# Optimization experiments

Hardware: AMD Instinct MI355X
Metric: run time of the kernel (lower is better)

Reference implementation:

```python
import jax, jax.numpy as jnp
import numpy as np

B, NQ, NN, EMB, H, D = 64, 256, 512, 128, 8, 16
SQRT_EMB = float(np.sqrt(EMB))
LOGIT_CLIP = 10.0


def setup_inputs() -> dict:
    key = jax.random.key(0)
    ks = jax.random.split(key, 9)
    encoded_last_node = jax.random.normal(ks[0], (B, NQ, EMB), jnp.float32)
    attr = jax.random.uniform(ks[1], (B, NQ, 1), jnp.float32)  # e.g. remaining load in [0,1]
    encoded_nodes = jax.random.normal(ks[2], (B, NN, EMB), jnp.float32)
    ninf_mask = jnp.where(jax.random.uniform(ks[3], (B, NQ, NN)) < 0.15,
                          -jnp.inf, 0.0).astype(jnp.float32)
    def lin(k, fan_in, fan_out):
        lim = 1.0 / np.sqrt(fan_in)
        return jax.random.uniform(k, (fan_in, fan_out), jnp.float32, -lim, lim)
    Wq_last = lin(ks[4], EMB + 1, H * D)
    Wk = lin(ks[5], EMB, H * D)
    Wv = lin(ks[6], EMB, H * D)
    Wcomb = lin(ks[7], H * D, EMB)
    bcomb = jax.random.uniform(ks[8], (EMB,), jnp.float32, -1.0 / np.sqrt(H * D), 1.0 / np.sqrt(H * D))
    return dict(encoded_last_node=encoded_last_node, attr=attr,
                encoded_nodes=encoded_nodes, ninf_mask=ninf_mask,
                Wq_last=Wq_last, Wk=Wk, Wv=Wv, Wcomb=Wcomb, bcomb=bcomb)


def _heads(x):  # [B, T, H*D] -> [B, H, T, D]
    return x.reshape(x.shape[0], x.shape[1], H, D).transpose(0, 2, 1, 3)


def reference(encoded_last_node, attr, encoded_nodes, ninf_mask,
              Wq_last, Wk, Wv, Wcomb, bcomb):
    # fix fully-masked rows: un-mask index 0 (matches torch mask_inf patch)
    all_inf = jnp.isinf(ninf_mask).all(axis=2)  # [B, NQ]
    ninf_mask = ninf_mask.at[:, :, 0].set(jnp.where(all_inf, 0.0, ninf_mask[:, :, 0]))

    # set_kv
    k = _heads(encoded_nodes @ Wk)  # [B,H,NN,D]
    v = _heads(encoded_nodes @ Wv)  # [B,H,NN,D]

    # q from last node + attr
    q = _heads(jnp.concatenate([encoded_last_node, attr], axis=2) @ Wq_last)  # [B,H,NQ,D]

    # masked multi-head attention
    score = jnp.einsum('bhnd,bhmd->bhnm', q, k) / jnp.sqrt(jnp.float32(D))
    score = score + ninf_mask[:, None, :, :]          # rank3 mask broadcast over heads
    weights = jax.nn.softmax(score, axis=-1)          # [B,H,NQ,NN]
    out = jnp.einsum('bhnm,bhmd->bhnd', weights, v)
    out_concat = out.transpose(0, 2, 1, 3).reshape(B, NQ, H * D)
    mh_atten_out = out_concat @ Wcomb + bcomb         # [B,NQ,EMB]

    # single-head compatibility score + tanh clip + mask + softmax
    score2 = jnp.einsum('bne,bme->bnm', mh_atten_out, encoded_nodes) / SQRT_EMB
    logits = LOGIT_CLIP * jnp.tanh(score2) + ninf_mask
    probs = jax.nn.softmax(logits, axis=2)            # [B,NQ,NN]
    return probs
```

## Files before the change

kernel.cpp:

```cpp
#include <hip/hip_runtime.h>
#include <math.h>

#define NB    64
#define NQn   256
#define NNn   512
#define HDn   128
#define LOG2E 1.44269504088896340736f
#define INV_SQRT_EMB 0.08838834764831845f

__device__ __forceinline__ float4 ldg4(const float* p) {
    return *reinterpret_cast<const float4*>(p);
}

__global__ __launch_bounds__(256, 2)
void proj_kernel(const float* __restrict__ X,
                 const float* __restrict__ W0, const float* __restrict__ W1,
                 const float* __restrict__ wrow, const float* __restrict__ attr,
                 const float* __restrict__ bias,
                 float* __restrict__ Y0, float* __restrict__ Y1)
{
    __shared__ float Xs[64 * 128];
    __shared__ float Wt[64 * 128];
    const int tid = threadIdx.x;
    const int rg = tid >> 4;
    const int cg = tid & 15;
    const int rowblk = blockIdx.x * 64;
    const int colbase = blockIdx.y * 64;

    #pragma unroll
    for (int i = 0; i < 8; ++i) {
        int idx = tid + 256 * i;
        int r = idx >> 5;
        int c4 = idx & 31;
        float4 v = ldg4(X + (rowblk + r) * 128 + c4 * 4);
        *reinterpret_cast<float4*>(&Xs[r * 128 + ((c4 ^ (r & 7)) << 2)]) = v;
    }

    for (int pass = 0; pass < 2; ++pass) {
        if (pass && (W1 == nullptr)) break;
        const float* W = pass ? W1 : W0;
        float* Y = pass ? Y1 : Y0;
        __syncthreads();
        #pragma unroll
        for (int i = 0; i < 32; ++i) {
            int idx = tid + 256 * i;
            int k = idx >> 6;
            int c = idx & 63;
            float w = W[k * 128 + colbase + c];
            Wt[c * 128 + ((((k >> 2) ^ (c & 7)) << 2) | (k & 3))] = w;
        }
        __syncthreads();

        float acc[4][4];
        #pragma unroll
        for (int r = 0; r < 4; ++r)
            #pragma unroll
            for (int c = 0; c < 4; ++c) acc[r][c] = 0.f;

        const int rsw = rg & 7;
        const int csw = cg & 7;
        #pragma unroll 8
        for (int k4 = 0; k4 < 32; ++k4) {
            float4 a[4], bv[4];
            #pragma unroll
            for (int r = 0; r < 4; ++r)
                a[r] = *reinterpret_cast<const float4*>(&Xs[(rg + 16 * r) * 128 + ((k4 ^ rsw) << 2)]);
            #pragma unroll
            for (int c = 0; c < 4; ++c)
                bv[c] = *reinterpret_cast<const float4*>(&Wt[(cg + 16 * c) * 128 + ((k4 ^ csw) << 2)]);
            #pragma unroll
            for (int r = 0; r < 4; ++r)
                #pragma unroll
                for (int c = 0; c < 4; ++c)
                    acc[r][c] += a[r].x * bv[c].x + a[r].y * bv[c].y
                               + a[r].z * bv[c].z + a[r].w * bv[c].w;
        }

        if (attr != nullptr) {
            #pragma unroll
            for (int r = 0; r < 4; ++r) {
                float av = attr[rowblk + rg + 16 * r];
                #pragma unroll
                for (int c = 0; c < 4; ++c)
                    acc[r][c] += av * wrow[colbase + cg + 16 * c];
            }
        }
        #pragma unroll
        for (int r = 0; r < 4; ++r) {
            int row = rowblk + rg + 16 * r;
            #pragma unroll
            for (int c = 0; c < 4; ++c) {
                int col = colbase + cg + 16 * c;
                float o = acc[r][c];
                if (bias != nullptr) o += bias[col];
                Y[row * 128 + col] = o;
            }
        }
    }
}

__global__ __launch_bounds__(512, 4)
void attn_kernel(const float* __restrict__ Q, const float* __restrict__ K,
                 const float* __restrict__ V, const float* __restrict__ mask,
                 float* __restrict__ P0, float* __restrict__ P1,
                 float* __restrict__ L0, float* __restrict__ L1)
{
    __shared__ float Ks[32 * 128];
    __shared__ float Vs[32 * 128];
    __shared__ float Ms[32 * 64];
    const int tid  = threadIdx.x;
    const int lane = tid & 63;
    const int h    = tid >> 6;
    const int b    = blockIdx.x;
    const int qt   = blockIdx.y;
    const int ns   = blockIdx.z;
    const int q    = qt * 64 + lane;
    const int nb   = ns * 256;

    float qv[16];
    {
        const float* qp = Q + (b * NQn + q) * 128 + h * 16;
        const float sc = 0.25f * LOG2E;
        float4 t0 = ldg4(qp), t1 = ldg4(qp + 4), t2 = ldg4(qp + 8), t3 = ldg4(qp + 12);
        qv[0]=t0.x*sc;  qv[1]=t0.y*sc;  qv[2]=t0.z*sc;  qv[3]=t0.w*sc;
        qv[4]=t1.x*sc;  qv[5]=t1.y*sc;  qv[6]=t1.z*sc;  qv[7]=t1.w*sc;
        qv[8]=t2.x*sc;  qv[9]=t2.y*sc;  qv[10]=t2.z*sc; qv[11]=t2.w*sc;
        qv[12]=t3.x*sc; qv[13]=t3.y*sc; qv[14]=t3.z*sc; qv[15]=t3.w*sc;
    }

    float out[16];
    #pragma unroll
    for (int d = 0; d < 16; ++d) out[d] = 0.f;
    float lsum = 0.f;

    const int srow = tid >> 3;
    const int sn4  = tid & 7;

    for (int t = 0; t < 8; ++t) {
        const int n0 = nb + t * 32;
        __syncthreads();
        {
            int i0 = tid, i1 = tid + 512;
            const float* kg = K + (b * NNn + n0) * 128;
            const float* vg = V + (b * NNn + n0) * 128;
            float4 k0 = ldg4(kg + i0 * 4), k1 = ldg4(kg + i1 * 4);
            float4 v0 = ldg4(vg + i0 * 4), v1 = ldg4(vg + i1 * 4);
            float4 mk = ldg4(mask + (b * NQn + qt * 64 + srow) * NNn + n0 + sn4 * 4);
            *reinterpret_cast<float4*>(&Ks[i0 * 4]) = k0;
            *reinterpret_cast<float4*>(&Ks[i1 * 4]) = k1;
            *reinterpret_cast<float4*>(&Vs[i0 * 4]) = v0;
            *reinterpret_cast<float4*>(&Vs[i1 * 4]) = v1;
            float mks[4] = {mk.x, mk.y, mk.z, mk.w};
            #pragma unroll
            for (int j = 0; j < 4; ++j) {
                int n = sn4 * 4 + j;
                Ms[n * 64 + (srow ^ n)] = mks[j];
            }
        }
        __syncthreads();

        const float* kbase = &Ks[h * 16];
        const float* vbase = &Vs[h * 16];
        #pragma unroll 2
        for (int g = 0; g < 8; ++g) {
            float p[4];
            #pragma unroll
            for (int j = 0; j < 4; ++j) {
                const int n = g * 4 + j;
                const float* kr = kbase + n * 128;
                float kf[16];
                *reinterpret_cast<float4*>(&kf[0])  = *reinterpret_cast<const float4*>(kr);
                *reinterpret_cast<float4*>(&kf[4])  = *reinterpret_cast<const float4*>(kr + 4);
                *reinterpret_cast<float4*>(&kf[8])  = *reinterpret_cast<const float4*>(kr + 8);
                *reinterpret_cast<float4*>(&kf[12]) = *reinterpret_cast<const float4*>(kr + 12);
                float mv = Ms[n * 64 + (lane ^ n)];
                float sA = qv[0]*kf[0] + qv[1]*kf[1] + qv[2]*kf[2] + qv[3]*kf[3];
                float sB = qv[4]*kf[4] + qv[5]*kf[5] + qv[6]*kf[6] + qv[7]*kf[7];
                float sC = qv[8]*kf[8] + qv[9]*kf[9] + qv[10]*kf[10] + qv[11]*kf[11];
                float sD = qv[12]*kf[12] + qv[13]*kf[13] + qv[14]*kf[14] + qv[15]*kf[15];
                float s = ((sA + sB) + (sC + sD)) + mv;
                p[j] = exp2f(s);
                lsum += p[j];
            }
            #pragma unroll
            for (int j = 0; j < 4; ++j) {
                const int n = g * 4 + j;
                const float* vr = vbase + n * 128;
                float vf[16];
                *reinterpret_cast<float4*>(&vf[0])  = *reinterpret_cast<const float4*>(vr);
                *reinterpret_cast<float4*>(&vf[4])  = *reinterpret_cast<const float4*>(vr + 4);
                *reinterpret_cast<float4*>(&vf[8])  = *reinterpret_cast<const float4*>(vr + 8);
                *reinterpret_cast<float4*>(&vf[12]) = *reinterpret_cast<const float4*>(vr + 12);
                #pragma unroll
                for (int d = 0; d < 16; ++d) out[d] += p[j] * vf[d];
            }
        }
    }

    float* P = ns ? P1 : P0;
    float* L = ns ? L1 : L0;
    float* op = P + (b * NQn + q) * 128 + h * 16;
    *reinterpret_cast<float4*>(op)      = make_float4(out[0],  out[1],  out[2],  out[3]);
    *reinterpret_cast<float4*>(op + 4)  = make_float4(out[4],  out[5],  out[6],  out[7]);
    *reinterpret_cast<float4*>(op + 8)  = make_float4(out[8],  out[9],  out[10], out[11]);
    *reinterpret_cast<float4*>(op + 12) = make_float4(out[12], out[13], out[14], out[15]);
    L[(b * NQn + q) * 8 + h] = lsum;
}

__global__ __launch_bounds__(256, 4)
void attn_merge(const float* __restrict__ P0, const float* __restrict__ P1,
                const float* __restrict__ L0, const float* __restrict__ L1,
                const float* __restrict__ V, float* __restrict__ ATT)
{
    const int idx = blockIdx.x * 256 + threadIdx.x;
    const int row = idx >> 5;
    const int f4i = idx & 31;
    const int hh  = f4i >> 2;
    const int b   = row >> 8;
    const float l = L0[row * 8 + hh] + L1[row * 8 + hh];
    float4 a = ldg4(P0 + row * 128 + f4i * 4);
    float4 c = ldg4(P1 + row * 128 + f4i * 4);
    float4 r;
    if (l == 0.0f) {
        r = ldg4(V + (size_t)b * NNn * 128 + f4i * 4);
    } else {
        float inv = __builtin_amdgcn_rcpf(l);
        r = make_float4((a.x + c.x) * inv, (a.y + c.y) * inv,
                        (a.z + c.z) * inv, (a.w + c.w) * inv);
    }
    *reinterpret_cast<float4*>(ATT + row * 128 + f4i * 4) = r;
}

__global__ __launch_bounds__(512, 2)
void final_kernel(const float* __restrict__ MH, const float* __restrict__ EN,
                  const float* __restrict__ mask, float* __restrict__ OUT)
{
    __shared__ float ENs[128 * 128];
    const int tid = threadIdx.x;
    const int qg = tid >> 4;
    const int mg = tid & 15;
    const int b  = blockIdx.x >> 2;
    const int q0 = (blockIdx.x & 3) * 64;

    const float* mhbase = MH + (b * NQn + q0) * 128;
    float pr[2][32];
    float psum[2] = {0.f, 0.f};
    const int msw = mg & 7;

    #pragma unroll
    for (int t = 0; t < 4; ++t) {
        const int m0 = t * 128;
        __syncthreads();
        #pragma unroll
        for (int i = 0; i < 8; ++i) {
            int idx = tid + 512 * i;
            int r = idx >> 5;
            int c4 = idx & 31;
            float4 v = ldg4(EN + (b * NNn + m0 + r) * 128 + c4 * 4);
            *reinterpret_cast<float4*>(&ENs[r * 128 + ((c4 ^ (r & 7)) << 2)]) = v;
        }
        __syncthreads();

        float acc[2][8];
        #pragma unroll
        for (int qq = 0; qq < 2; ++qq)
            #pragma unroll
            for (int c = 0; c < 8; ++c) acc[qq][c] = 0.f;

        #pragma unroll 4
        for (int k4 = 0; k4 < 32; ++k4) {
            float4 a0 = ldg4(mhbase + (qg * 2 + 0) * 128 + k4 * 4);
            float4 a1 = ldg4(mhbase + (qg * 2 + 1) * 128 + k4 * 4);
            float4 bv[8];
            #pragma unroll
            for (int c = 0; c < 8; ++c)
                bv[c] = *reinterpret_cast<const float4*>(&ENs[(mg + 16 * c) * 128 + ((k4 ^ msw) << 2)]);
            #pragma unroll
            for (int c = 0; c < 8; ++c) {
                acc[0][c] += a0.x*bv[c].x + a0.y*bv[c].y + a0.z*bv[c].z + a0.w*bv[c].w;
                acc[1][c] += a1.x*bv[c].x + a1.y*bv[c].y + a1.z*bv[c].z + a1.w*bv[c].w;
            }
        }

        #pragma unroll
        for (int qq = 0; qq < 2; ++qq) {
            const int q = q0 + qg * 2 + qq;
            const float* mrow = mask + (b * NQn + q) * NNn + m0;
            #pragma unroll
            for (int c = 0; c < 8; ++c) {
                int m = mg + 16 * c;
                float s2 = acc[qq][c] * INV_SQRT_EMB;
                float e  = exp2f(s2 * (2.0f * LOG2E));
                float rc = __builtin_amdgcn_rcpf(e + 1.0f);
                float mv = mrow[m];
                float pv = exp2f((mv - 20.0f * rc) * LOG2E);
                pr[qq][t * 8 + c] = pv;
                psum[qq] += pv;
            }
        }
    }

    #pragma unroll
    for (int qq = 0; qq < 2; ++qq) {
        float s = psum[qq];
        s += __shfl_xor(s, 1);
        s += __shfl_xor(s, 2);
        s += __shfl_xor(s, 4);
        s += __shfl_xor(s, 8);
        psum[qq] = s;
    }

    #pragma unroll
    for (int qq = 0; qq < 2; ++qq) {
        const int q = q0 + qg * 2 + qq;
        float* orow = OUT + (b * NQn + q) * NNn;
        if (psum[qq] == 0.0f) {
            #pragma unroll
            for (int t = 0; t < 4; ++t)
                #pragma unroll
                for (int c = 0; c < 8; ++c) {
                    int m = t * 128 + mg + 16 * c;
                    orow[m] = (m == 0) ? 1.0f : 0.0f;
                }
        } else {
            float inv = __builtin_amdgcn_rcpf(psum[qq]);
            #pragma unroll
            for (int t = 0; t < 4; ++t)
                #pragma unroll
                for (int c = 0; c < 8; ++c)
                    orow[t * 128 + mg + 16 * c] = pr[qq][t * 8 + c] * inv;
        }
    }
}

extern "C" void kernel_launch(void* const* d_in, const int* in_sizes, int n_in,
                              void* d_out, int out_size, void* d_ws, size_t ws_size,
                              hipStream_t stream) {
    const float* enc_last  = (const float*)d_in[0];
    const float* attr      = (const float*)d_in[1];
    const float* enc_nodes = (const float*)d_in[2];
    const float* mask      = (const float*)d_in[3];
    const float* Wq        = (const float*)d_in[4];
    const float* Wk        = (const float*)d_in[5];
    const float* Wv        = (const float*)d_in[6];
    const float* Wcomb     = (const float*)d_in[7];
    const float* bcomb     = (const float*)d_in[8];
    float* out = (float*)d_out;

    float* Kbuf = (float*)d_ws;
    float* Vbuf = Kbuf + (size_t)NB * NNn * 128;
    float* Qbuf = Vbuf + (size_t)NB * NNn * 128;
    float* ATT  = Qbuf + (size_t)NB * NQn * 128;
    float* MH   = ATT  + (size_t)NB * NQn * 128;
    float* P1   = MH   + (size_t)NB * NQn * 128;
    float* L0   = P1   + (size_t)NB * NQn * 128;
    float* L1   = L0   + (size_t)NB * NQn * 8;

    proj_kernel<<<dim3(NB * NNn / 64, 2), 256, 0, stream>>>(
        enc_nodes, Wk, Wv, nullptr, nullptr, nullptr, Kbuf, Vbuf);
    proj_kernel<<<dim3(NB * NQn / 64, 2), 256, 0, stream>>>(
        enc_last, Wq, nullptr, Wq + 128 * 128, attr, nullptr, Qbuf, nullptr);
    attn_kernel<<<dim3(NB, 4, 2), 512, 0, stream>>>(
        Qbuf, Kbuf, Vbuf, mask, ATT, P1, L0, L1);
    attn_merge<<<dim3(NB * NQn * 32 / 256), 256, 0, stream>>>(
        ATT, P1, L0, L1, Vbuf, ATT);
    proj_kernel<<<dim3(NB * NQn / 64, 2), 256, 0, stream>>>(
        ATT, Wcomb, nullptr, nullptr, nullptr, bcomb, MH, nullptr);
    final_kernel<<<dim3(NB * NQn / 64), 512, 0, stream>>>(
        MH, enc_nodes, mask, out);
}
```

Before: 245.2 us.

## Shrink per-thread tiles in projection and final kernels, restructure attention inner loop

The projection kernel moves to 512 threads per block with a 2x4 register tile instead of 4x4. The final kernel gives each thread one query row instead of two and launches twice as many blocks. The attention inner loop now processes key/value pairs two at a time with fused score and accumulate steps instead of groups of four. The aim is more resident waves to hide latency, at the cost of less register reuse and more shared-memory and global loads per FLOP (the final kernel loads encoded_nodes into LDS twice as many times).

```diff
diff --git a/kernel.cpp b/kernel.cpp
--- a/kernel.cpp
+++ b/kernel.cpp
@@ -12,7 +12,7 @@
     return *reinterpret_cast<const float4*>(p);
 }
 
-__global__ __launch_bounds__(256, 2)
+__global__ __launch_bounds__(512, 4)
 void proj_kernel(const float* __restrict__ X,
                  const float* __restrict__ W0, const float* __restrict__ W1,
                  const float* __restrict__ wrow, const float* __restrict__ attr,
@@ -28,8 +28,8 @@
     const int colbase = blockIdx.y * 64;
 
     #pragma unroll
-    for (int i = 0; i < 8; ++i) {
-        int idx = tid + 256 * i;
+    for (int i = 0; i < 4; ++i) {
+        int idx = tid + 512 * i;
         int r = idx >> 5;
         int c4 = idx & 31;
         float4 v = ldg4(X + (rowblk + r) * 128 + c4 * 4);
@@ -42,8 +42,8 @@
         float* Y = pass ? Y1 : Y0;
         __syncthreads();
         #pragma unroll
-        for (int i = 0; i < 32; ++i) {
-            int idx = tid + 256 * i;
+        for (int i = 0; i < 16; ++i) {
+            int idx = tid + 512 * i;
             int k = idx >> 6;
             int c = idx & 63;
             float w = W[k * 128 + colbase + c];
@@ -51,9 +51,9 @@
         }
         __syncthreads();
 
-        float acc[4][4];
-        #pragma unroll
-        for (int r = 0; r < 4; ++r)
+        float acc[2][4];
+        #pragma unroll
+        for (int r = 0; r < 2; ++r)
             #pragma unroll
             for (int c = 0; c < 4; ++c) acc[r][c] = 0.f;
 
@@ -61,15 +61,15 @@
         const int csw = cg & 7;
         #pragma unroll 8
         for (int k4 = 0; k4 < 32; ++k4) {
-            float4 a[4], bv[4];
-            #pragma unroll
-            for (int r = 0; r < 4; ++r)
-                a[r] = *reinterpret_cast<const float4*>(&Xs[(rg + 16 * r) * 128 + ((k4 ^ rsw) << 2)]);
+            float4 a[2], bv[4];
+            #pragma unroll
+            for (int r = 0; r < 2; ++r)
+                a[r] = *reinterpret_cast<const float4*>(&Xs[(rg + 32 * r) * 128 + ((k4 ^ rsw) << 2)]);
             #pragma unroll
             for (int c = 0; c < 4; ++c)
                 bv[c] = *reinterpret_cast<const float4*>(&Wt[(cg + 16 * c) * 128 + ((k4 ^ csw) << 2)]);
             #pragma unroll
-            for (int r = 0; r < 4; ++r)
+            for (int r = 0; r < 2; ++r)
                 #pragma unroll
                 for (int c = 0; c < 4; ++c)
                     acc[r][c] += a[r].x * bv[c].x + a[r].y * bv[c].y
@@ -78,16 +78,16 @@
 
         if (attr != nullptr) {
             #pragma unroll
-            for (int r = 0; r < 4; ++r) {
-                float av = attr[rowblk + rg + 16 * r];
+            for (int r = 0; r < 2; ++r) {
+                float av = attr[rowblk + rg + 32 * r];
                 #pragma unroll
                 for (int c = 0; c < 4; ++c)
                     acc[r][c] += av * wrow[colbase + cg + 16 * c];
             }
         }
         #pragma unroll
-        for (int r = 0; r < 4; ++r) {
-            int row = rowblk + rg + 16 * r;
+        for (int r = 0; r < 2; ++r) {
+            int row = rowblk + rg + 32 * r;
             #pragma unroll
             for (int c = 0; c < 4; ++c) {
                 int col = colbase + cg + 16 * c;
@@ -161,39 +161,51 @@
 
         const float* kbase = &Ks[h * 16];
         const float* vbase = &Vs[h * 16];
-        #pragma unroll 2
-        for (int g = 0; g < 8; ++g) {
-            float p[4];
-            #pragma unroll
-            for (int j = 0; j < 4; ++j) {
-                const int n = g * 4 + j;
-                const float* kr = kbase + n * 128;
-                float kf[16];
-                *reinterpret_cast<float4*>(&kf[0])  = *reinterpret_cast<const float4*>(kr);
-                *reinterpret_cast<float4*>(&kf[4])  = *reinterpret_cast<const float4*>(kr + 4);
-                *reinterpret_cast<float4*>(&kf[8])  = *reinterpret_cast<const float4*>(kr + 8);
-                *reinterpret_cast<float4*>(&kf[12]) = *reinterpret_cast<const float4*>(kr + 12);
-                float mv = Ms[n * 64 + (lane ^ n)];
-                float sA = qv[0]*kf[0] + qv[1]*kf[1] + qv[2]*kf[2] + qv[3]*kf[3];
-                float sB = qv[4]*kf[4] + qv[5]*kf[5] + qv[6]*kf[6] + qv[7]*kf[7];
-                float sC = qv[8]*kf[8] + qv[9]*kf[9] + qv[10]*kf[10] + qv[11]*kf[11];
-                float sD = qv[12]*kf[12] + qv[13]*kf[13] + qv[14]*kf[14] + qv[15]*kf[15];
-                float s = ((sA + sB) + (sC + sD)) + mv;
-                p[j] = exp2f(s);
-                lsum += p[j];
-            }
-            #pragma unroll
-            for (int j = 0; j < 4; ++j) {
-                const int n = g * 4 + j;
-                const float* vr = vbase + n * 128;
-                float vf[16];
-                *reinterpret_cast<float4*>(&vf[0])  = *reinterpret_cast<const float4*>(vr);
-                *reinterpret_cast<float4*>(&vf[4])  = *reinterpret_cast<const float4*>(vr + 4);
-                *reinterpret_cast<float4*>(&vf[8])  = *reinterpret_cast<const float4*>(vr + 8);
-                *reinterpret_cast<float4*>(&vf[12]) = *reinterpret_cast<const float4*>(vr + 12);
-                #pragma unroll
-                for (int d = 0; d < 16; ++d) out[d] += p[j] * vf[d];
-            }
+        for (int g = 0; g < 16; ++g) {
+            const int nA = g * 2, nB = g * 2 + 1;
+            const float* krA = kbase + nA * 128;
+            const float* krB = kbase + nB * 128;
+            const float* vrA = vbase + nA * 128;
+            const float* vrB = vbase + nB * 128;
+            float4 ka0 = *reinterpret_cast<const float4*>(krA);
+            float4 ka1 = *reinterpret_cast<const float4*>(krA + 4);
+            float4 ka2 = *reinterpret_cast<const float4*>(krA + 8);
+            float4 ka3 = *reinterpret_cast<const float4*>(krA + 12);
+            float4 kb0 = *reinterpret_cast<const float4*>(krB);
+            float4 kb1 = *reinterpret_cast<const float4*>(krB + 4);
+            float4 kb2 = *reinterpret_cast<const float4*>(krB + 8);
+            float4 kb3 = *reinterpret_cast<const float4*>(krB + 12);
+            float4 va0 = *reinterpret_cast<const float4*>(vrA);
+            float4 va1 = *reinterpret_cast<const float4*>(vrA + 4);
+            float4 va2 = *reinterpret_cast<const float4*>(vrA + 8);
+            float4 va3 = *reinterpret_cast<const float4*>(vrA + 12);
+            float4 vb0 = *reinterpret_cast<const float4*>(vrB);
+            float4 vb1 = *reinterpret_cast<const float4*>(vrB + 4);
+            float4 vb2 = *reinterpret_cast<const float4*>(vrB + 8);
+            float4 vb3 = *reinterpret_cast<const float4*>(vrB + 12);
+            float mvA = Ms[nA * 64 + (lane ^ nA)];
+            float mvB = Ms[nB * 64 + (lane ^ nB)];
+            float aP = qv[0]*ka0.x + qv[1]*ka0.y + qv[2]*ka0.z + qv[3]*ka0.w;
+            float aQ = qv[4]*ka1.x + qv[5]*ka1.y + qv[6]*ka1.z + qv[7]*ka1.w;
+            float aR = qv[8]*ka2.x + qv[9]*ka2.y + qv[10]*ka2.z + qv[11]*ka2.w;
+            float aS = qv[12]*ka3.x + qv[13]*ka3.y + qv[14]*ka3.z + qv[15]*ka3.w;
+            float bP = qv[0]*kb0.x + qv[1]*kb0.y + qv[2]*kb0.z + qv[3]*kb0.w;
+            float bQ = qv[4]*kb1.x + qv[5]*kb1.y + qv[6]*kb1.z + qv[7]*kb1.w;
+            float bR = qv[8]*kb2.x + qv[9]*kb2.y + qv[10]*kb2.z + qv[11]*kb2.w;
+            float bS = qv[12]*kb3.x + qv[13]*kb3.y + qv[14]*kb3.z + qv[15]*kb3.w;
+            float sA = ((aP + aQ) + (aR + aS)) + mvA;
+            float sB = ((bP + bQ) + (bR + bS)) + mvB;
+            float pA = exp2f(sA);
+            float pB = exp2f(sB);
+            lsum += pA + pB;
+            out[0]  += pA*va0.x + pB*vb0.x;  out[1]  += pA*va0.y + pB*vb0.y;
+            out[2]  += pA*va0.z + pB*vb0.z;  out[3]  += pA*va0.w + pB*vb0.w;
+            out[4]  += pA*va1.x + pB*vb1.x;  out[5]  += pA*va1.y + pB*vb1.y;
+            out[6]  += pA*va1.z + pB*vb1.z;  out[7]  += pA*va1.w + pB*vb1.w;
+            out[8]  += pA*va2.x + pB*vb2.x;  out[9]  += pA*va2.y + pB*vb2.y;
+            out[10] += pA*va2.z + pB*vb2.z;  out[11] += pA*va2.w + pB*vb2.w;
+            out[12] += pA*va3.x + pB*vb3.x;  out[13] += pA*va3.y + pB*vb3.y;
+            out[14] += pA*va3.z + pB*vb3.z;  out[15] += pA*va3.w + pB*vb3.w;
         }
     }
 
@@ -231,7 +243,7 @@
     *reinterpret_cast<float4*>(ATT + row * 128 + f4i * 4) = r;
 }
 
-__global__ __launch_bounds__(512, 2)
+__global__ __launch_bounds__(512, 4)
 void final_kernel(const float* __restrict__ MH, const float* __restrict__ EN,
                   const float* __restrict__ mask, float* __restrict__ OUT)
 {
@@ -239,12 +251,12 @@
     const int tid = threadIdx.x;
     const int qg = tid >> 4;
     const int mg = tid & 15;
-    const int b  = blockIdx.x >> 2;
-    const int q0 = (blockIdx.x & 3) * 64;
-
-    const float* mhbase = MH + (b * NQn + q0) * 128;
-    float pr[2][32];
-    float psum[2] = {0.f, 0.f};
+    const int b  = blockIdx.x >> 3;
+    const int q0 = (blockIdx.x & 7) * 32;
+
+    const float* mhrow = MH + (b * NQn + q0 + qg) * 128;
+    float pr[32];
+    float psum = 0.f;
     const int msw = mg & 7;
 
     #pragma unroll
@@ -261,75 +273,61 @@
         }
         __syncthreads();
 
-        float acc[2][8];
-        #pragma unroll
-        for (int qq = 0; qq < 2; ++qq)
-            #pragma unroll
-            for (int c = 0; c < 8; ++c) acc[qq][c] = 0.f;
+        float acc[8];
+        #pragma unroll
+        for (int c = 0; c < 8; ++c) acc[c] = 0.f;
 
         #pragma unroll 4
         for (int k4 = 0; k4 < 32; ++k4) {
-            float4 a0 = ldg4(mhbase + (qg * 2 + 0) * 128 + k4 * 4);
-            float4 a1 = ldg4(mhbase + (qg * 2 + 1) * 128 + k4 * 4);
+            float4 a0 = ldg4(mhrow + k4 * 4);
             float4 bv[8];
             #pragma unroll
             for (int c = 0; c < 8; ++c)
                 bv[c] = *reinterpret_cast<const float4*>(&ENs[(mg + 16 * c) * 128 + ((k4 ^ msw) << 2)]);
             #pragma unroll
-            for (int c = 0; c < 8; ++c) {
-                acc[0][c] += a0.x*bv[c].x + a0.y*bv[c].y + a0.z*bv[c].z + a0.w*bv[c].w;
-                acc[1][c] += a1.x*bv[c].x + a1.y*bv[c].y + a1.z*bv[c].z + a1.w*bv[c].w;
-            }
-        }
-
-        #pragma unroll
-        for (int qq = 0; qq < 2; ++qq) {
-            const int q = q0 + qg * 2 + qq;
-            const float* mrow = mask + (b * NQn + q) * NNn + m0;
-            #pragma unroll
-            for (int c = 0; c < 8; ++c) {
-                int m = mg + 16 * c;
-                float s2 = acc[qq][c] * INV_SQRT_EMB;
-                float e  = exp2f(s2 * (2.0f * LOG2E));
-                float rc = __builtin_amdgcn_rcpf(e + 1.0f);
-                float mv = mrow[m];
-                float pv = exp2f((mv - 20.0f * rc) * LOG2E);
-                pr[qq][t * 8 + c] = pv;
-                psum[qq] += pv;
-            }
-        }
-    }
-
-    #pragma unroll
-    for (int qq = 0; qq < 2; ++qq) {
-        float s = psum[qq];
+            for (int c = 0; c < 8; ++c)
+                acc[c] += a0.x*bv[c].x + a0.y*bv[c].y + a0.z*bv[c].z + a0.w*bv[c].w;
+        }
+
+        const float* mrow = mask + (b * NQn + q0 + qg) * NNn + m0;
+        #pragma unroll
+        for (int c = 0; c < 8; ++c) {
+            int m = mg + 16 * c;
+            float s2 = acc[c] * INV_SQRT_EMB;
+            float e  = exp2f(s2 * (2.0f * LOG2E));
+            float rc = __builtin_amdgcn_rcpf(e + 1.0f);
+            float mv = mrow[m];
+            float pv = exp2f((mv - 20.0f * rc) * LOG2E);
+            pr[t * 8 + c] = pv;
+            psum += pv;
+        }
+    }
+
+    {
+        float s = psum;
         s += __shfl_xor(s, 1);
         s += __shfl_xor(s, 2);
         s += __shfl_xor(s, 4);
         s += __shfl_xor(s, 8);
-        psum[qq] = s;
-    }
-
-    #pragma unroll
-    for (int qq = 0; qq < 2; ++qq) {
-        const int q = q0 + qg * 2 + qq;
-        float* orow = OUT + (b * NQn + q) * NNn;
-        if (psum[qq] == 0.0f) {
-            #pragma unroll
-            for (int t = 0; t < 4; ++t)
-                #pragma unroll
-                for (int c = 0; c < 8; ++c) {
-                    int m = t * 128 + mg + 16 * c;
-                    orow[m] = (m == 0) ? 1.0f : 0.0f;
-                }
-        } else {
-            float inv = __builtin_amdgcn_rcpf(psum[qq]);
-            #pragma unroll
-            for (int t = 0; t < 4; ++t)
-                #pragma unroll
-                for (int c = 0; c < 8; ++c)
-                    orow[t * 128 + mg + 16 * c] = pr[qq][t * 8 + c] * inv;
-        }
+        psum = s;
+    }
+
+    float* orow = OUT + (b * NQn + q0 + qg) * NNn;
+    if (psum == 0.0f) {
+        #pragma unroll
+        for (int t = 0; t < 4; ++t)
+            #pragma unroll
+            for (int c = 0; c < 8; ++c) {
+                int m = t * 128 + mg + 16 * c;
+                orow[m] = (m == 0) ? 1.0f : 0.0f;
+            }
+    } else {
+        float inv = __builtin_amdgcn_rcpf(psum);
+        #pragma unroll
+        for (int t = 0; t < 4; ++t)
+            #pragma unroll
+            for (int c = 0; c < 8; ++c)
+                orow[t * 128 + mg + 16 * c] = pr[t * 8 + c] * inv;
     }
 }
 
@@ -356,16 +354,16 @@
     float* L0   = P1   + (size_t)NB * NQn * 128;
     float* L1   = L0   + (size_t)NB * NQn * 8;
 
-    proj_kernel<<<dim3(NB * NNn / 64, 2), 256, 0, stream>>>(
+    proj_kernel<<<dim3(NB * NNn / 64, 2), 512, 0, stream>>>(
         enc_nodes, Wk, Wv, nullptr, nullptr, nullptr, Kbuf, Vbuf);
-    proj_kernel<<<dim3(NB * NQn / 64, 2), 256, 0, stream>>>(
+    proj_kernel<<<dim3(NB * NQn / 64, 2), 512, 0, stream>>>(
         enc_last, Wq, nullptr, Wq + 128 * 128, attr, nullptr, Qbuf, nullptr);
     attn_kernel<<<dim3(NB, 4, 2), 512, 0, stream>>>(
         Qbuf, Kbuf, Vbuf, mask, ATT, P1, L0, L1);
     attn_merge<<<dim3(NB * NQn * 32 / 256), 256, 0, stream>>>(
         ATT, P1, L0, L1, Vbuf, ATT);
-    proj_kernel<<<dim3(NB * NQn / 64, 2), 256, 0, stream>>>(
+    proj_kernel<<<dim3(NB * NQn / 64, 2), 512, 0, stream>>>(
         ATT, Wcomb, nullptr, nullptr, nullptr, bcomb, MH, nullptr);
-    final_kernel<<<dim3(NB * NQn / 64), 512, 0, stream>>>(
+    final_kernel<<<dim3(NB * NQn / 32), 512, 0, stream>>>(
         MH, enc_nodes, mask, out);
 }
```

Measured after the change: 267.2 us. +9.0%, slower.
